# Optimization experiments

Measured on AMD Instinct MI355X. Metric: run time of the kernel, lower is better.

## Reference

```python
import jax, jax.numpy as jnp
import numpy as np

L, C = 256, 20
BATCH = 1024


def _pairwise_mask(L, C, mask_type='pairwise'):
    # mask[l1, c1, l2, c2] nonzero iff positions interact (l2 - l1 >= 1, or == 1 for neighbor)
    ls = jnp.arange(L)
    d = ls[None, :] - ls[:, None]  # [L, L] = l2 - l1
    m = (d >= 1) if mask_type == 'pairwise' else (d == 1)
    return jnp.broadcast_to(m[:, None, :, None], (L, C, L, C)).astype(jnp.float32)


def setup_inputs() -> dict:
    key = jax.random.key(0)
    k1, k2, k3 = jax.random.split(key, 3)
    x_lc = jax.random.uniform(k1, (BATCH, L * C), dtype=jnp.float32)
    theta_0 = jnp.zeros((1,), dtype=jnp.float32)
    theta_lc = jax.random.normal(k2, (L, C), dtype=jnp.float32) / np.sqrt(L)
    theta_lclc = jax.random.normal(k3, (L, C, L, C), dtype=jnp.float32) / np.sqrt(L * L)
    return {"x_lc": x_lc, "theta_0": theta_0, "theta_lc": theta_lc, "theta_lclc": theta_lclc}


def reference(x_lc, theta_0, theta_lc, theta_lclc):
    Ld, Cd = theta_lc.shape
    mask = _pairwise_mask(Ld, Cd, 'pairwise')
    # additive term: sum_lc theta_lc * x_lc  -> [B, 1]
    lin = x_lc @ theta_lc.reshape(Ld * Cd)  # [B]
    # pairwise term: x^T (theta * mask) x, expressed as a masked GEMM instead of a
    # broadcasted [B, L, C, L, C] product
    Theta = (theta_lclc * mask).reshape(Ld * Cd, Ld * Cd)  # [LC, LC]
    xm = x_lc @ Theta  # [B, LC]
    quad = jnp.sum(xm * x_lc, axis=1)  # [B]
    phi = theta_0 + (lin + quad)[:, None]  # [B, 1]
    return phi
```

## Files before the change

kernel.cpp:

```cpp
#include <hip/hip_runtime.h>
#include <hip/hip_bf16.h>
#include <cstdint>
#include <cstddef>

#define LCN 5120
#define BN  1024
#define CN  20
#define TP  65

typedef __attribute__((ext_vector_type(4))) float  floatx4;
typedef __attribute__((ext_vector_type(8))) short  shortx8;
typedef __attribute__((ext_vector_type(4))) unsigned short ushortx4;
typedef __attribute__((ext_vector_type(8))) unsigned short ushortx8;

static __device__ __forceinline__ unsigned short f2bf(float f) {
    __hip_bfloat16 h = __float2bfloat16(f);
    return *reinterpret_cast<unsigned short*>(&h);
}

static __device__ __forceinline__ void gload_lds16(const void* g, void* l) {
    __builtin_amdgcn_global_load_lds(
        (const __attribute__((address_space(1))) void*)g,
        (__attribute__((address_space(3))) void*)l,
        16, 0, 0);
}

__global__ __launch_bounds__(256) void k_theta(const float* __restrict__ th,
                                               unsigned short* __restrict__ Tt) {
    const int i0 = blockIdx.x * 64;
    const int j0 = blockIdx.y * 64;
    const int lmax = (128 * (i0 / 128) + 127) / CN;
    const int ch   = (CN * lmax + 511) / 512;
    if (j0 >= ch * 512) return;

    __shared__ unsigned short Ts[64 * TP];
    const int t = threadIdx.x;
    const int c = t & 15, r = t >> 4;
#pragma unroll
    for (int rr = 0; rr < 4; ++rr) {
        const int j  = j0 + rr * 16 + r;
        const int lj = j / CN;
        const floatx4 v = *reinterpret_cast<const floatx4*>(th + (size_t)j * LCN + i0 + c * 4);
#pragma unroll
        for (int e = 0; e < 4; ++e) {
            const int li = (i0 + c * 4 + e) / CN;
            Ts[(rr * 16 + r) * TP + c * 4 + e] = (li > lj) ? f2bf(v[e]) : (unsigned short)0;
        }
    }
    __syncthreads();
    const int c2 = t & 7, r2 = t >> 3;
#pragma unroll
    for (int ww = 0; ww < 2; ++ww) {
        const int il = ww * 32 + r2;
        ushortx8 o;
#pragma unroll
        for (int e = 0; e < 8; ++e) o[e] = Ts[(c2 * 8 + e) * TP + il];
        *reinterpret_cast<ushortx8*>(Tt + (size_t)(i0 + il) * LCN + j0 + c2 * 8) = o;
    }
}

__global__ __launch_bounds__(256) void k_init(const float* __restrict__ x,
                                              const float* __restrict__ th0,
                                              const float* __restrict__ thlc,
                                              float* __restrict__ out,
                                              unsigned short* __restrict__ Xb) {
    const int b = blockIdx.x;
    const int tid = threadIdx.x;
    const floatx4* xr = reinterpret_cast<const floatx4*>(x + (size_t)b * LCN);
    const floatx4* tr = reinterpret_cast<const floatx4*>(thlc);
    ushortx4* xw = reinterpret_cast<ushortx4*>(Xb + (size_t)b * LCN);
    float s = 0.0f;
    for (int k = tid; k < LCN / 4; k += 256) {
        const floatx4 a = xr[k], t2 = tr[k];
        s += a[0] * t2[0] + a[1] * t2[1] + a[2] * t2[2] + a[3] * t2[3];
        ushortx4 o;
#pragma unroll
        for (int e = 0; e < 4; ++e) o[e] = f2bf(a[e]);
        xw[k] = o;
    }
#pragma unroll
    for (int off = 32; off > 0; off >>= 1) s += __shfl_down(s, off, 64);
    __shared__ float ws4[4];
    if ((tid & 63) == 0) ws4[tid >> 6] = s;
    __syncthreads();
    if (tid == 0) out[b] = th0[0] + ws4[0] + ws4[1] + ws4[2] + ws4[3];
}

__global__ __launch_bounds__(256) void k_quad(
    const unsigned short* __restrict__ Xb,
    const unsigned short* __restrict__ Tt,
    float*                __restrict__ out,
    const int tot)
{
    const int bid  = blockIdx.x;
    const int xcd  = bid & 7;
    const int slot = bid >> 3;
    const int m    = slot & 7;
    const int g    = slot >> 3;
    int q = g * 8 + xcd;
    if (q >= tot) return;

    __shared__ unsigned short As[128 * 32];
    __shared__ unsigned short Bs[128 * 32];
    __shared__ float partial[128];

    const int tid  = threadIdx.x;
    const int lane = tid & 63;
    const int w    = tid >> 6;
    const int wm   = w & 1;
    const int wn   = w >> 1;
    const int lrow = lane & 15;
    const int kq   = lane >> 4;

    int n = 0, c = 0;
    for (int t = 0; t < 40; ++t) {
        const int lmax = (128 * t + 127) / CN;
        const int chn  = (CN * lmax + 511) / 512;
        if (q < chn) { n = t; c = q; break; }
        q -= chn;
    }
    const int b0 = m * 128;
    const int n0 = n * 128;
    const int k0 = c * 512;

    if (tid < 128) partial[tid] = 0.0f;

    floatx4 acc[4][4];
#pragma unroll
    for (int mt = 0; mt < 4; ++mt)
#pragma unroll
        for (int nt = 0; nt < 4; ++nt) acc[mt][nt] = (floatx4)0.0f;

    int aoff[4], boff[4];
#pragma unroll
    for (int mt = 0; mt < 4; ++mt) {
        const int row = wm * 64 + mt * 16 + lrow;
        aoff[mt] = row * 32 + (((kq + (row >> 1)) & 3) << 3);
    }
#pragma unroll
    for (int nt = 0; nt < 4; ++nt) {
        const int row = wn * 64 + nt * 16 + lrow;
        boff[nt] = row * 32 + (((kq + (row >> 1)) & 3) << 3);
    }

    for (int kk = 0; kk < 16; ++kk) {
        const int kc = k0 + kk * 32;
#pragma unroll
        for (int t = 0; t < 2; ++t) {
            const int s    = t * 256 + tid;
            const int row  = s >> 2;
            const int gseg = ((s & 3) - (row >> 1)) & 3;
            char* la = (char*)As + (size_t)(t * 256 + w * 64) * 16;
            char* lb = (char*)Bs + (size_t)(t * 256 + w * 64) * 16;
            gload_lds16(Xb + (size_t)(b0 + row) * LCN + kc + gseg * 8, la);
            gload_lds16(Tt + (size_t)(n0 + row) * LCN + kc + gseg * 8, lb);
        }
        __syncthreads();

        shortx8 af[4], bfr[4];
#pragma unroll
        for (int mt = 0; mt < 4; ++mt)
            af[mt] = *reinterpret_cast<const shortx8*>(As + aoff[mt]);
#pragma unroll
        for (int nt = 0; nt < 4; ++nt)
            bfr[nt] = *reinterpret_cast<const shortx8*>(Bs + boff[nt]);
#pragma unroll
        for (int mt = 0; mt < 4; ++mt)
#pragma unroll
            for (int nt = 0; nt < 4; ++nt)
                acc[mt][nt] = __builtin_amdgcn_mfma_f32_16x16x32_bf16(af[mt], bfr[nt], acc[mt][nt], 0, 0, 0);
        __syncthreads();
    }

#pragma unroll
    for (int mt = 0; mt < 4; ++mt) {
#pragma unroll
        for (int r = 0; r < 4; ++r) {
            const int b = b0 + wm * 64 + mt * 16 + kq * 4 + r;
            float s = 0.0f;
#pragma unroll
            for (int nt = 0; nt < 4; ++nt) {
                const int i = n0 + wn * 64 + nt * 16 + lrow;
                const __hip_bfloat16 hv = *reinterpret_cast<const __hip_bfloat16*>(&Xb[(size_t)b * LCN + i]);
                s += acc[mt][nt][r] * __bfloat162float(hv);
            }
            s += __shfl_xor(s, 1, 64);
            s += __shfl_xor(s, 2, 64);
            s += __shfl_xor(s, 4, 64);
            s += __shfl_xor(s, 8, 64);
            if (lrow == 0) atomicAdd(&partial[b - b0], s);
        }
    }
    __syncthreads();
    if (tid < 128) atomicAdd(&out[b0 + tid], partial[tid]);
}

extern "C" void kernel_launch(void* const* d_in, const int* in_sizes, int n_in,
                              void* d_out, int out_size, void* d_ws, size_t ws_size,
                              hipStream_t stream) {
    const float* x      = (const float*)d_in[0];
    const float* th0    = (const float*)d_in[1];
    const float* thlc   = (const float*)d_in[2];
    const float* thlclc = (const float*)d_in[3];
    float* out = (float*)d_out;

    unsigned short* Tt = (unsigned short*)d_ws;
    unsigned short* Xb = (unsigned short*)((char*)d_ws + (size_t)LCN * LCN * 2);

    k_theta<<<dim3(LCN / 64, LCN / 64), 256, 0, stream>>>(thlclc, Tt);
    k_init<<<dim3(BN), 256, 0, stream>>>(x, th0, thlc, out, Xb);

    int tot = 0;
    for (int t = 0; t < 40; ++t) {
        const int lmax = (128 * t + 127) / CN;
        tot += (CN * lmax + 511) / 512;
    }
    const int groups = (tot + 7) / 8;
    k_quad<<<dim3(groups * 64), 256, 0, stream>>>(Xb, Tt, out, tot);
}
```

Baseline: 234.4 us.

## Drop theta transpose, use row-major masked bf16 theta and fuse prep kernels

The theta preparation no longer transposes through shared memory. It converts each row of theta to bf16 in row-major order, zeroes masked entries, and writes only the nonzero region, which lets the GEMM index the upper triangle by row instead of column. The theta conversion and the x conversion plus linear term are merged into one launch, saving a kernel launch and removing the LDS transpose. The quad kernel's tile enumeration is redone to match the new triangular layout, which changes the set of K chunks each tile visits.

```diff
diff --git a/kernel.cpp b/kernel.cpp
--- a/kernel.cpp
+++ b/kernel.cpp
@@ -6,7 +6,6 @@
 #define LCN 5120
 #define BN  1024
 #define CN  20
-#define TP  65
 
 typedef __attribute__((ext_vector_type(4))) float  floatx4;
 typedef __attribute__((ext_vector_type(8))) short  shortx8;
@@ -25,70 +24,60 @@
         16, 0, 0);
 }
 
-__global__ __launch_bounds__(256) void k_theta(const float* __restrict__ th,
-                                               unsigned short* __restrict__ Tt) {
-    const int i0 = blockIdx.x * 64;
-    const int j0 = blockIdx.y * 64;
-    const int lmax = (128 * (i0 / 128) + 127) / CN;
-    const int ch   = (CN * lmax + 511) / 512;
-    if (j0 >= ch * 512) return;
-
-    __shared__ unsigned short Ts[64 * TP];
-    const int t = threadIdx.x;
-    const int c = t & 15, r = t >> 4;
-#pragma unroll
-    for (int rr = 0; rr < 4; ++rr) {
-        const int j  = j0 + rr * 16 + r;
-        const int lj = j / CN;
-        const floatx4 v = *reinterpret_cast<const floatx4*>(th + (size_t)j * LCN + i0 + c * 4);
-#pragma unroll
-        for (int e = 0; e < 4; ++e) {
-            const int li = (i0 + c * 4 + e) / CN;
-            Ts[(rr * 16 + r) * TP + c * 4 + e] = (li > lj) ? f2bf(v[e]) : (unsigned short)0;
-        }
-    }
-    __syncthreads();
-    const int c2 = t & 7, r2 = t >> 3;
-#pragma unroll
-    for (int ww = 0; ww < 2; ++ww) {
-        const int il = ww * 32 + r2;
-        ushortx8 o;
-#pragma unroll
-        for (int e = 0; e < 8; ++e) o[e] = Ts[(c2 * 8 + e) * TP + il];
-        *reinterpret_cast<ushortx8*>(Tt + (size_t)(i0 + il) * LCN + j0 + c2 * 8) = o;
-    }
-}
-
-__global__ __launch_bounds__(256) void k_init(const float* __restrict__ x,
-                                              const float* __restrict__ th0,
-                                              const float* __restrict__ thlc,
-                                              float* __restrict__ out,
-                                              unsigned short* __restrict__ Xb) {
-    const int b = blockIdx.x;
+__global__ __launch_bounds__(256) void k_prep(
+    const float* __restrict__ th,
+    const float* __restrict__ x,
+    const float* __restrict__ th0,
+    const float* __restrict__ thlc,
+    unsigned short* __restrict__ Tb,
+    unsigned short* __restrict__ Xb,
+    float*          __restrict__ out)
+{
     const int tid = threadIdx.x;
-    const floatx4* xr = reinterpret_cast<const floatx4*>(x + (size_t)b * LCN);
-    const floatx4* tr = reinterpret_cast<const floatx4*>(thlc);
-    ushortx4* xw = reinterpret_cast<ushortx4*>(Xb + (size_t)b * LCN);
-    float s = 0.0f;
-    for (int k = tid; k < LCN / 4; k += 256) {
-        const floatx4 a = xr[k], t2 = tr[k];
-        s += a[0] * t2[0] + a[1] * t2[1] + a[2] * t2[2] + a[3] * t2[3];
-        ushortx4 o;
-#pragma unroll
-        for (int e = 0; e < 4; ++e) o[e] = f2bf(a[e]);
-        xw[k] = o;
-    }
-#pragma unroll
-    for (int off = 32; off > 0; off >>= 1) s += __shfl_down(s, off, 64);
-    __shared__ float ws4[4];
-    if ((tid & 63) == 0) ws4[tid >> 6] = s;
-    __syncthreads();
-    if (tid == 0) out[b] = th0[0] + ws4[0] + ws4[1] + ws4[2] + ws4[3];
+    if (blockIdx.x < LCN / 4) {
+        const int w = tid >> 6, lane = tid & 63;
+        const int i = blockIdx.x * 4 + w;
+        const int lmin = ((i >> 7) << 7) / CN;
+        const int js   = 512 * ((CN * (lmin + 1)) / 512);
+        const int jmin = CN * (i / CN) + CN;
+        const float* src = th + (size_t)i * LCN;
+        unsigned short* dst = Tb + (size_t)i * LCN;
+        for (int j = js + lane * 8; j < LCN; j += 512) {
+            const floatx4 v0 = *reinterpret_cast<const floatx4*>(src + j);
+            const floatx4 v1 = *reinterpret_cast<const floatx4*>(src + j + 4);
+            ushortx8 o;
+#pragma unroll
+            for (int e = 0; e < 4; ++e) o[e]     = (j + e     >= jmin) ? f2bf(v0[e]) : (unsigned short)0;
+#pragma unroll
+            for (int e = 0; e < 4; ++e) o[4 + e] = (j + 4 + e >= jmin) ? f2bf(v1[e]) : (unsigned short)0;
+            *reinterpret_cast<ushortx8*>(dst + j) = o;
+        }
+    } else {
+        const int b = blockIdx.x - LCN / 4;
+        const floatx4* xr = reinterpret_cast<const floatx4*>(x + (size_t)b * LCN);
+        const floatx4* tr = reinterpret_cast<const floatx4*>(thlc);
+        ushortx4* xw = reinterpret_cast<ushortx4*>(Xb + (size_t)b * LCN);
+        float s = 0.0f;
+        for (int k = tid; k < LCN / 4; k += 256) {
+            const floatx4 a = xr[k], t2 = tr[k];
+            s += a[0] * t2[0] + a[1] * t2[1] + a[2] * t2[2] + a[3] * t2[3];
+            ushortx4 o;
+#pragma unroll
+            for (int e = 0; e < 4; ++e) o[e] = f2bf(a[e]);
+            xw[k] = o;
+        }
+#pragma unroll
+        for (int off = 32; off > 0; off >>= 1) s += __shfl_down(s, off, 64);
+        __shared__ float ws4[4];
+        if ((tid & 63) == 0) ws4[tid >> 6] = s;
+        __syncthreads();
+        if (tid == 0) out[b] = th0[0] + ws4[0] + ws4[1] + ws4[2] + ws4[3];
+    }
 }
 
 __global__ __launch_bounds__(256) void k_quad(
     const unsigned short* __restrict__ Xb,
-    const unsigned short* __restrict__ Tt,
+    const unsigned short* __restrict__ Tb,
     float*                __restrict__ out,
     const int tot)
 {
@@ -114,10 +103,11 @@
 
     int n = 0, c = 0;
     for (int t = 0; t < 40; ++t) {
-        const int lmax = (128 * t + 127) / CN;
-        const int chn  = (CN * lmax + 511) / 512;
-        if (q < chn) { n = t; c = q; break; }
-        q -= chn;
+        const int lmin = (128 * t) / CN;
+        const int c0   = (CN * (lmin + 1)) / 512;
+        const int cnt  = 10 - c0;
+        if (q < cnt) { n = t; c = c0 + q; break; }
+        q -= cnt;
     }
     const int b0 = m * 128;
     const int n0 = n * 128;
@@ -153,7 +143,7 @@
             char* la = (char*)As + (size_t)(t * 256 + w * 64) * 16;
             char* lb = (char*)Bs + (size_t)(t * 256 + w * 64) * 16;
             gload_lds16(Xb + (size_t)(b0 + row) * LCN + kc + gseg * 8, la);
-            gload_lds16(Tt + (size_t)(n0 + row) * LCN + kc + gseg * 8, lb);
+            gload_lds16(Tb + (size_t)(n0 + row) * LCN + kc + gseg * 8, lb);
         }
         __syncthreads();
 
@@ -204,17 +194,17 @@
     const float* thlclc = (const float*)d_in[3];
     float* out = (float*)d_out;
 
-    unsigned short* Tt = (unsigned short*)d_ws;
+    unsigned short* Tb = (unsigned short*)d_ws;
     unsigned short* Xb = (unsigned short*)((char*)d_ws + (size_t)LCN * LCN * 2);
 
-    k_theta<<<dim3(LCN / 64, LCN / 64), 256, 0, stream>>>(thlclc, Tt);
-    k_init<<<dim3(BN), 256, 0, stream>>>(x, th0, thlc, out, Xb);
+    k_prep<<<dim3(LCN / 4 + BN), 256, 0, stream>>>(thlclc, x, th0, thlc, Tb, Xb, out);
 
     int tot = 0;
     for (int t = 0; t < 40; ++t) {
-        const int lmax = (128 * t + 127) / CN;
-        tot += (CN * lmax + 511) / 512;
+        const int lmin = (128 * t) / CN;
+        const int c0   = (CN * (lmin + 1)) / 512;
+        tot += 10 - c0;
     }
     const int groups = (tot + 7) / 8;
-    k_quad<<<dim3(groups * 64), 256, 0, stream>>>(Xb, Tt, out, tot);
-}
+    k_quad<<<dim3(groups * 64), 256, 0, stream>>>(Xb, Tb, out, tot);
+}
```

Measured after the change: 234.0 us. About the same (-0.2%).
